# Kernel optimization log

Hardware: AMD Instinct MI355X
Metric: run time of the kernel (lower is better)

The kernel has to match this reference:

```python
import jax, jax.numpy as jnp
import numpy as np

N, E, H, L, IN, OUT = 50000, 600000, 128, 4, 10, 3
EPS = 1e-5

def _ln(x, g, b):
    m = jnp.mean(x, axis=-1, keepdims=True)
    v = jnp.mean(jnp.square(x - m), axis=-1, keepdims=True)
    return (x - m) * jax.lax.rsqrt(v + EPS) * g + b

def _mlp(x, w1, b1, w2, b2, g, be):
    h = jax.nn.relu(x @ w1 + b1)
    return _ln(h @ w2 + b2, g, be)

def setup_inputs() -> dict:
    key = jax.random.key(0)
    ks = iter(jax.random.split(key, 40))
    def w(shape, fan_in):
        return jax.random.normal(next(ks), shape, jnp.float32) * (1.0 / np.sqrt(fan_in))
    inp = {
        'x': jax.random.normal(next(ks), (N, IN), jnp.float32),
        'edge_index': jax.random.randint(next(ks), (2, E), 0, N, jnp.int32),
        'edge_attr': jax.random.normal(next(ks), (E, 3), jnp.float32),
        'enc_w1': w((IN, H), IN), 'enc_b1': jnp.zeros((H,), jnp.float32),
        'enc_w2': w((H, H), H), 'enc_b2': jnp.zeros((H,), jnp.float32),
        'enc_g': jnp.ones((H,), jnp.float32), 'enc_be': jnp.zeros((H,), jnp.float32),
        'edge_w1': w((L, 2 * H + 3, H), 2 * H + 3), 'edge_b1': jnp.zeros((L, H), jnp.float32),
        'edge_w2': w((L, H, H), H), 'edge_b2': jnp.zeros((L, H), jnp.float32),
        'edge_g': jnp.ones((L, H), jnp.float32), 'edge_be': jnp.zeros((L, H), jnp.float32),
        'node_w1': w((L, 2 * H, H), 2 * H), 'node_b1': jnp.zeros((L, H), jnp.float32),
        'node_w2': w((L, H, H), H), 'node_b2': jnp.zeros((L, H), jnp.float32),
        'node_g': jnp.ones((L, H), jnp.float32), 'node_be': jnp.zeros((L, H), jnp.float32),
        'dec_w1': w((H, H), H), 'dec_b1': jnp.zeros((H,), jnp.float32),
        'dec_w2': w((H, OUT), H), 'dec_b2': jnp.zeros((OUT,), jnp.float32),
    }
    return inp

def reference(x, edge_index, edge_attr,
              enc_w1, enc_b1, enc_w2, enc_b2, enc_g, enc_be,
              edge_w1, edge_b1, edge_w2, edge_b2, edge_g, edge_be,
              node_w1, node_b1, node_w2, node_b2, node_g, node_be,
              dec_w1, dec_b1, dec_w2, dec_b2):
    src, tgt = edge_index[0], edge_index[1]  # x_j = h[src], x_i = h[tgt]
    h = _mlp(x, enc_w1, enc_b1, enc_w2, enc_b2, enc_g, enc_be)  # [N,H]
    for l in range(L):
        x_i, x_j = h[tgt], h[src]                               # [E,H] gathers
        msg_in = jnp.concatenate([x_i, x_j, edge_attr], axis=1)  # [E,2H+3]
        msg = _mlp(msg_in, edge_w1[l], edge_b1[l], edge_w2[l], edge_b2[l], edge_g[l], edge_be[l])
        aggr = jax.ops.segment_sum(msg, tgt, num_segments=h.shape[0])  # [N,H]
        upd_in = jnp.concatenate([h, aggr], axis=1)              # [N,2H]
        h = h + _mlp(upd_in, node_w1[l], node_b1[l], node_w2[l], node_b2[l], node_g[l], node_be[l])
    out = jax.nn.relu(h @ dec_w1 + dec_b1) @ dec_w2 + dec_b2     # [N,OUT]
    return out
```

## Files before the change

### kernel.cpp

```cpp
#include <hip/hip_runtime.h>

#define H 128
#define LPAD 132
#define BM 64

typedef __attribute__((ext_vector_type(8))) short bf8;
typedef __attribute__((ext_vector_type(4))) float f4;
typedef __attribute__((ext_vector_type(4))) short s4;

__device__ __forceinline__ short f2bf(float f) {
    unsigned u = __float_as_uint(f);
    unsigned r = u + 0x7FFFu + ((u >> 16) & 1u);
    return (short)(r >> 16);
}
__device__ __forceinline__ float bf2f(unsigned lo16) {
    return __uint_as_float((lo16 & 0xFFFFu) << 16);
}

__global__ void pack_w(const float* __restrict__ W, short* __restrict__ out, int K, int KC) {
    const int layer = blockIdx.z;
    const float* Wl = W + (size_t)layer * K * H;
    short* ol = out + (size_t)layer * 8 * KC * 512;
    const int total = 8 * KC * 512;
    for (int idx = blockIdx.x * blockDim.x + threadIdx.x; idx < total; idx += gridDim.x * blockDim.x) {
        int i = idx & 7;
        int lane = (idx >> 3) & 63;
        int v = idx >> 9;
        int kc = v % KC;
        int m = v / KC;
        int k = kc * 32 + (lane >> 4) * 8 + i;
        int c = m * 16 + (lane & 15);
        float val = (k < K) ? Wl[(size_t)k * H + c] : 0.f;
        ol[idx] = f2bf(val);
    }
}

__global__ void pack_wts(const float* __restrict__ W , short* __restrict__ out) {
    const int layer = blockIdx.z;
    const float* Wl = W + (size_t)layer * 259 * 128;
    short* ol = out + (size_t)layer * 16 * 4 * 512;
    const int total = 16 * 4 * 512;
    for (int idx = blockIdx.x * blockDim.x + threadIdx.x; idx < total; idx += gridDim.x * blockDim.x) {
        int i = idx & 7;
        int lane = (idx >> 3) & 63;
        int v = idx >> 9;
        int kc = v & 3;
        int m = v >> 2;
        int k = kc * 32 + (lane >> 4) * 8 + i;
        int c = m * 16 + (lane & 15);
        float val = (c < 128) ? Wl[(size_t)k * 128 + c] : Wl[(size_t)(128 + k) * 128 + (c - 128)];
        ol[idx] = f2bf(val);
    }
}

__global__ void csr_count(const int* __restrict__ tgt, int* __restrict__ cnt, int E) {
    int e = blockIdx.x * blockDim.x + threadIdx.x;
    if (e < E) atomicAdd(&cnt[tgt[e]], 1);
}

#define SCAN_T 1024
__global__ __launch_bounds__(SCAN_T) void scan_excl(const int* __restrict__ cnt,
                                                    int* __restrict__ start, int n) {
    __shared__ int part[SCAN_T];
    int t = threadIdx.x;
    int chunk = (n + SCAN_T - 1) / SCAN_T;
    int lo = t * chunk, hi = min(lo + chunk, n);
    int s = 0;
    for (int i = lo; i < hi; ++i) s += cnt[i];
    part[t] = s;
    __syncthreads();
    for (int off = 1; off < SCAN_T; off <<= 1) {
        int v = (t >= off) ? part[t - off] : 0;
        __syncthreads();
        part[t] += v;
        __syncthreads();
    }
    int base = (t > 0) ? part[t - 1] : 0;
    for (int i = lo; i < hi; ++i) { start[i] = base; base += cnt[i]; }
}

__global__ void csr_scatter_reorder(const int* __restrict__ tgtI, const int* __restrict__ srcI,
                                    const float* __restrict__ eattr,
                                    int* __restrict__ start,
                                    int* __restrict__ srcs, int* __restrict__ tgts,
                                    short* __restrict__ attrb, int E) {
    int e = blockIdx.x * blockDim.x + threadIdx.x;
    if (e >= E) return;
    int t = tgtI[e];
    int p = atomicAdd(&start[t], 1);
    srcs[p] = srcI[e];
    tgts[p] = t;
    bf8 vv = {};
    vv[0] = f2bf(eattr[(size_t)e * 3 + 0]);
    vv[1] = f2bf(eattr[(size_t)e * 3 + 1]);
    vv[2] = f2bf(eattr[(size_t)e * 3 + 2]);
    *(bf8*)(attrb + (size_t)p * 8) = vv;
}

__global__ __launch_bounds__(512, 4) void ts_mfma(
    const short* __restrict__ hbf, const short* __restrict__ wtsp,
    const float* __restrict__ b1, float* __restrict__ TS, int N) {
    __shared__ __align__(16) short sW[16 * 4 * 512];
    const int tid = threadIdx.x;
    for (int t = tid; t < 16 * 4 * 512 / 8; t += 512) ((uint4*)sW)[t] = ((const uint4*)wtsp)[t];
    __syncthreads();

    const int lane = tid & 63;
    const int wv = tid >> 6;
    const int g = lane >> 4;
    const int er = lane & 15;
    const int n = blockIdx.x * 128 + wv * 16 + er;
    const int nC = (n < N) ? n : 0;
    const bf8* rT = (const bf8*)(hbf + (size_t)nC * H);

    f4 acc[16] = {};
#pragma unroll
    for (int kc = 0; kc < 4; ++kc) {
        bf8 b = rT[kc * 4 + g];
#pragma unroll
        for (int m = 0; m < 16; ++m)
            acc[m] = __builtin_amdgcn_mfma_f32_16x16x32_bf16(
                *(const bf8*)(sW + ((m * 4 + kc) * 64 + lane) * 8), b, acc[m], 0, 0, 0);
    }
    if (n >= N) return;
    float* o = TS + (size_t)n * 256;
#pragma unroll
    for (int m = 0; m < 16; ++m) {
        f4 v = acc[m];
        if (m < 8) {
            f4 bb = *(const f4*)(b1 + m * 16 + 4 * g);
            v = v + bb;
        }
        *(f4*)(o + m * 16 + 4 * g) = v;
    }
}

__global__ __launch_bounds__(512, 4) void edge_fused(
    const float* __restrict__ TS,
    const short* __restrict__ attrbf,
    const int* __restrict__ srcs, const int* __restrict__ tgts,
    const short* __restrict__ w2p,
    const float* __restrict__ w1aG,
    const float* __restrict__ b2,
    const float* __restrict__ gamma, const float* __restrict__ beta,
    float* __restrict__ aggr, int nrows) {
    __shared__ __align__(16) short sW2[8 * 4 * 512];
    __shared__ float sw1a[3 * 128];
    __shared__ __align__(16) unsigned smsg[128 * 64];
    __shared__ int stgt[128];

    const int tid = threadIdx.x;
    for (int t = tid; t < 8 * 4 * 512 / 8; t += 512) ((uint4*)sW2)[t] = ((const uint4*)w2p)[t];
    if (tid < 384) sw1a[tid] = w1aG[tid];
    const int e0b = blockIdx.x * 128;
    if (tid < 128) {
        int ee = e0b + tid;
        stgt[tid] = (ee < nrows) ? tgts[ee] : -1;
    }
    __syncthreads();

    const int lane = tid & 63;
    const int wv = tid >> 6;
    const int g = lane >> 4;
    const int er = lane & 15;
    const int le = wv * 16 + er;
    const int e = e0b + le;
    const bool valid = e < nrows;
    const int eC = valid ? e : 0;
    const int tS = srcs[eC];
    const int tT = tgts[eC];

    uint2 au = *(const uint2*)(attrbf + (size_t)eC * 8);
    const float at0 = bf2f(au.x), at1 = bf2f(au.x >> 16), at2 = bf2f(au.y);

    const float* Tp = TS + (size_t)tT * 256;
    const float* Sp = TS + (size_t)tS * 256 + 128;

    f4 acc2[8] = {};
#pragma unroll
    for (int kc2 = 0; kc2 < 4; ++kc2) {
        const int c0 = kc2 * 32 + 8 * g;
        f4 t0 = *(const f4*)(Tp + c0);
        f4 t1 = *(const f4*)(Tp + c0 + 4);
        f4 s0 = *(const f4*)(Sp + c0);
        f4 s1 = *(const f4*)(Sp + c0 + 4);
        float hv[8];
#pragma unroll
        for (int r = 0; r < 4; ++r) {
            float a = t0[r] + s0[r] + at0 * sw1a[c0 + r] + at1 * sw1a[128 + c0 + r] + at2 * sw1a[256 + c0 + r];
            hv[r] = fmaxf(a, 0.f);
            float b = t1[r] + s1[r] + at0 * sw1a[c0 + 4 + r] + at1 * sw1a[128 + c0 + 4 + r] + at2 * sw1a[256 + c0 + 4 + r];
            hv[4 + r] = fmaxf(b, 0.f);
        }
        bf8 bfr;
        unsigned* bu = (unsigned*)&bfr;
#pragma unroll
        for (int p = 0; p < 4; ++p)
            asm("v_cvt_pk_bf16_f32 %0, %1, %2" : "=v"(bu[p]) : "v"(hv[2 * p]), "v"(hv[2 * p + 1]));
#pragma unroll
        for (int m = 0; m < 8; ++m)
            acc2[m] = __builtin_amdgcn_mfma_f32_16x16x32_bf16(
                *(const bf8*)(sW2 + ((m * 4 + kc2) * 64 + lane) * 8), bfr, acc2[m], 0, 0, 0);
    }

    float o[8][4];
    float s = 0.f, q = 0.f;
#pragma unroll
    for (int m = 0; m < 8; ++m) {
        f4 bb = *(const f4*)(b2 + m * 16 + 4 * g);
#pragma unroll
        for (int r = 0; r < 4; ++r) {
            float v = acc2[m][r] + bb[r];
            o[m][r] = v; s += v; q += v * v;
        }
    }
    s += __shfl_xor(s, 16, 64); q += __shfl_xor(q, 16, 64);
    s += __shfl_xor(s, 32, 64); q += __shfl_xor(q, 32, 64);
    const float mean = s * (1.f / 128.f);
    const float inv = rsqrtf(q * (1.f / 128.f) - mean * mean + 1e-5f);

    const unsigned swz = (unsigned)((le & 7) << 3);
    unsigned* row = smsg + le * 64;
#pragma unroll
    for (int m = 0; m < 8; ++m) {
        f4 gg = *(const f4*)(gamma + m * 16 + 4 * g);
        f4 be4 = *(const f4*)(beta + m * 16 + 4 * g);
        float v0 = valid ? ((o[m][0] - mean) * inv * gg[0] + be4[0]) : 0.f;
        float v1 = valid ? ((o[m][1] - mean) * inv * gg[1] + be4[1]) : 0.f;
        float v2 = valid ? ((o[m][2] - mean) * inv * gg[2] + be4[2]) : 0.f;
        float v3 = valid ? ((o[m][3] - mean) * inv * gg[3] + be4[3]) : 0.f;
        unsigned p0, p1;
        asm("v_cvt_pk_bf16_f32 %0, %1, %2" : "=v"(p0) : "v"(v0), "v"(v1));
        asm("v_cvt_pk_bf16_f32 %0, %1, %2" : "=v"(p1) : "v"(v2), "v"(v3));
        unsigned d0 = ((unsigned)(m * 8 + 2 * g)) ^ swz;
        uint2 uu; uu.x = p0; uu.y = p1;
        *(uint2*)(row + d0) = uu;
    }
    __syncthreads();

    const int c2 = tid & 63;
    const int chunk = tid >> 6;
    float a0 = 0.f, a1 = 0.f;
    int cur = stgt[chunk * 16];
    for (int j = 0; j < 16; ++j) {
        int le2 = chunk * 16 + j;
        int tg = stgt[le2];
        if (tg != cur) {
            if (cur >= 0) {
                atomicAdd(&aggr[(size_t)cur * 128 + 2 * c2], a0);
                atomicAdd(&aggr[(size_t)cur * 128 + 2 * c2 + 1], a1);
            }
            a0 = 0.f; a1 = 0.f; cur = tg;
        }
        unsigned u = smsg[le2 * 64 + (c2 ^ ((le2 & 7) << 3))];
        a0 += __uint_as_float(u << 16);
        a1 += __uint_as_float(u & 0xFFFF0000u);
    }
    if (cur >= 0) {
        atomicAdd(&aggr[(size_t)cur * 128 + 2 * c2], a0);
        atomicAdd(&aggr[(size_t)cur * 128 + 2 * c2 + 1], a1);
    }
}

__global__ __launch_bounds__(1024, 4) void node_mfma(
    const short* __restrict__ hbf, const float* __restrict__ aggrf,
    const short* __restrict__ w1p, const short* __restrict__ w2p,
    const float* __restrict__ b1, const float* __restrict__ b2,
    const float* __restrict__ gamma, const float* __restrict__ beta,
    float* __restrict__ outp, short* __restrict__ hbfout, int nrows) {
    __shared__ __align__(16) short sW1[8 * 8 * 512];
    __shared__ __align__(16) short sW2[8 * 4 * 512];

    const int tid = threadIdx.x;
    for (int t = tid; t < 8 * 8 * 512 / 8; t += 1024) ((uint4*)sW1)[t] = ((const uint4*)w1p)[t];
    for (int t = tid; t < 8 * 4 * 512 / 8; t += 1024) ((uint4*)sW2)[t] = ((const uint4*)w2p)[t];
    __syncthreads();

    const int lane = tid & 63;
    const int wv = tid >> 6;
    const int g = lane >> 4;
    const int er = lane & 15;
    const int e = blockIdx.x * 256 + wv * 16 + er;
    const bool valid = e < nrows;
    const int eC = valid ? e : 0;

    const bf8* rT = (const bf8*)(hbf + (size_t)eC * H);
    const f4* ra = (const f4*)(aggrf + (size_t)eC * H);

    f4 acc1[8] = {};
#pragma unroll
    for (int kc = 0; kc < 4; ++kc) {
        bf8 b = rT[kc * 4 + g];
#pragma unroll
        for (int m = 0; m < 8; ++m)
            acc1[m] = __builtin_amdgcn_mfma_f32_16x16x32_bf16(
                *(const bf8*)(sW1 + ((m * 8 + kc) * 64 + lane) * 8), b, acc1[m], 0, 0, 0);
    }
#pragma unroll
    for (int kc = 4; kc < 8; ++kc) {
        f4 a0 = ra[(kc - 4) * 8 + g * 2];
        f4 a1 = ra[(kc - 4) * 8 + g * 2 + 1];
        bf8 b;
        unsigned* bu = (unsigned*)&b;
        asm("v_cvt_pk_bf16_f32 %0, %1, %2" : "=v"(bu[0]) : "v"(a0[0]), "v"(a0[1]));
        asm("v_cvt_pk_bf16_f32 %0, %1, %2" : "=v"(bu[1]) : "v"(a0[2]), "v"(a0[3]));
        asm("v_cvt_pk_bf16_f32 %0, %1, %2" : "=v"(bu[2]) : "v"(a1[0]), "v"(a1[1]));
        asm("v_cvt_pk_bf16_f32 %0, %1, %2" : "=v"(bu[3]) : "v"(a1[2]), "v"(a1[3]));
#pragma unroll
        for (int m = 0; m < 8; ++m)
            acc1[m] = __builtin_amdgcn_mfma_f32_16x16x32_bf16(
                *(const bf8*)(sW1 + ((m * 8 + kc) * 64 + lane) * 8), b, acc1[m], 0, 0, 0);
    }

    float h1[8][4];
#pragma unroll
    for (int m = 0; m < 8; ++m) {
        f4 bb = *(const f4*)(b1 + m * 16 + 4 * g);
#pragma unroll
        for (int r = 0; r < 4; ++r) h1[m][r] = fmaxf(acc1[m][r] + bb[r], 0.f);
    }

    unsigned pk[8][2];
#pragma unroll
    for (int m = 0; m < 8; ++m)
#pragma unroll
        for (int hh = 0; hh < 2; ++hh)
            asm("v_cvt_pk_bf16_f32 %0, %1, %2"
                : "=v"(pk[m][hh]) : "v"(h1[m][2 * hh]), "v"(h1[m][2 * hh + 1]));

    f4 acc2[8] = {};
#pragma unroll
    for (int kc2 = 0; kc2 < 4; ++kc2) {
        bf8 bfr;
        unsigned* bu = (unsigned*)&bfr;
#pragma unroll
        for (int p = 0; p < 4; ++p) {
            int sl = er + 16 * (2 * (g & 1) + (p >> 1));
            unsigned lo = (unsigned)__shfl((int)pk[2 * kc2 + 0][p & 1], sl, 64);
            unsigned hi = (unsigned)__shfl((int)pk[2 * kc2 + 1][p & 1], sl, 64);
            bu[p] = (g >> 1) ? hi : lo;
        }
#pragma unroll
        for (int m = 0; m < 8; ++m)
            acc2[m] = __builtin_amdgcn_mfma_f32_16x16x32_bf16(
                *(const bf8*)(sW2 + ((m * 4 + kc2) * 64 + lane) * 8), bfr, acc2[m], 0, 0, 0);
    }

    float o[8][4];
    float s = 0.f, q = 0.f;
#pragma unroll
    for (int m = 0; m < 8; ++m) {
        f4 bb = *(const f4*)(b2 + m * 16 + 4 * g);
#pragma unroll
        for (int r = 0; r < 4; ++r) {
            float v = acc2[m][r] + bb[r];
            o[m][r] = v; s += v; q += v * v;
        }
    }
    s += __shfl_xor(s, 16, 64); q += __shfl_xor(q, 16, 64);
    s += __shfl_xor(s, 32, 64); q += __shfl_xor(q, 32, 64);
    const float mean = s * (1.f / 128.f);
    const float inv = rsqrtf(q * (1.f / 128.f) - mean * mean + 1e-5f);

    if (!valid) return;
    float* hp = outp + (size_t)eC * H;
    short* hb = hbfout + (size_t)eC * H;
#pragma unroll
    for (int m = 0; m < 8; ++m) {
        f4 gg = *(const f4*)(gamma + m * 16 + 4 * g);
        f4 be4 = *(const f4*)(beta + m * 16 + 4 * g);
        f4 hv = *(const f4*)(hp + m * 16 + 4 * g);
        f4 nv; s4 pkk;
#pragma unroll
        for (int r = 0; r < 4; ++r) {
            nv[r] = hv[r] + (o[m][r] - mean) * inv * gg[r] + be4[r];
            pkk[r] = f2bf(nv[r]);
        }
        *(f4*)(hp + m * 16 + 4 * g) = nv;
        *(s4*)(hb + m * 16 + 4 * g) = pkk;
    }
}

enum { MODE_ENC = 0, MODE_DEC = 3 };

__device__ __forceinline__ void fma_row(float acc[4], float a, const float4& b) {
    acc[0] = fmaf(a, b.x, acc[0]);
    acc[1] = fmaf(a, b.y, acc[1]);
    acc[2] = fmaf(a, b.z, acc[2]);
    acc[3] = fmaf(a, b.w, acc[3]);
}

__device__ __forceinline__ void gemm_seg(const float (*A)[LPAD], int K,
                                         const float* __restrict__ B,
                                         int row0, int c0, float acc[8][4]) {
    int k = 0;
    for (; k + 4 <= K; k += 4) {
        float4 b0 = *(const float4*)(B + (size_t)(k + 0) * H + c0);
        float4 b1 = *(const float4*)(B + (size_t)(k + 1) * H + c0);
        float4 b2 = *(const float4*)(B + (size_t)(k + 2) * H + c0);
        float4 b3 = *(const float4*)(B + (size_t)(k + 3) * H + c0);
#pragma unroll
        for (int j = 0; j < 8; ++j) {
            float4 a = *(const float4*)(&A[row0 + j][k]);
            fma_row(acc[j], a.x, b0);
            fma_row(acc[j], a.y, b1);
            fma_row(acc[j], a.z, b2);
            fma_row(acc[j], a.w, b3);
        }
    }
    for (; k < K; ++k) {
        float4 bv = *(const float4*)(B + (size_t)k * H + c0);
#pragma unroll
        for (int j = 0; j < 8; ++j) fma_row(acc[j], A[row0 + j][k], bv);
    }
}

template <int MODE>
__global__ __launch_bounds__(256, 2) void mlp_small(
    const float* __restrict__ in0,
    const float* __restrict__ w1, const float* __restrict__ b1,
    const float* __restrict__ w2, const float* __restrict__ b2,
    const float* __restrict__ g, const float* __restrict__ be,
    float* __restrict__ outp, short* __restrict__ hbfout, int nrows) {
    __shared__ __align__(16) float sA[BM][LPAD];

    const int tid = threadIdx.x;
    const int tr = tid >> 5, tc = tid & 31;
    const int c0 = tc * 4, row0 = tr * 8;
    const int r0 = blockIdx.x * BM;

    if (MODE == MODE_ENC) {
        for (int idx = tid; idx < BM * 10; idx += 256) {
            int r = idx / 10, c = idx - 10 * (idx / 10);
            int n = r0 + r;
            sA[r][c] = (n < nrows) ? in0[(size_t)n * 10 + c] : 0.f;
        }
    } else {
        for (int idx = tid; idx < BM * 32; idx += 256) {
            int r = idx >> 5, qq = idx & 31;
            int n = r0 + r;
            float4 v0 = make_float4(0.f, 0.f, 0.f, 0.f);
            if (n < nrows) v0 = ((const float4*)in0)[(size_t)n * 32 + qq];
            *(float4*)&sA[r][qq * 4] = v0;
        }
    }
    __syncthreads();

    float acc[8][4];
    {
        float4 bb = *(const float4*)&b1[c0];
#pragma unroll
        for (int j = 0; j < 8; ++j) { acc[j][0] = bb.x; acc[j][1] = bb.y; acc[j][2] = bb.z; acc[j][3] = bb.w; }
    }
    gemm_seg(sA, (MODE == MODE_ENC) ? 10 : H, w1, row0, c0, acc);
#pragma unroll
    for (int j = 0; j < 8; ++j)
#pragma unroll
        for (int r = 0; r < 4; ++r) acc[j][r] = fmaxf(acc[j][r], 0.f);

    __syncthreads();
#pragma unroll
    for (int j = 0; j < 8; ++j)
        *(float4*)&sA[row0 + j][c0] = make_float4(acc[j][0], acc[j][1], acc[j][2], acc[j][3]);
    __syncthreads();

    if (MODE == MODE_DEC) {
        if (tid < BM * 3) {
            int r = tid / 3, o = tid - 3 * (tid / 3);
            int gr = r0 + r;
            float sv = b2[o];
            for (int i = 0; i < H; ++i) sv = fmaf(sA[r][i], w2[(size_t)i * 3 + o], sv);
            if (gr < nrows) outp[(size_t)gr * 3 + o] = sv;
        }
        return;
    }

    {
        float4 bb = *(const float4*)&b2[c0];
#pragma unroll
        for (int j = 0; j < 8; ++j) { acc[j][0] = bb.x; acc[j][1] = bb.y; acc[j][2] = bb.z; acc[j][3] = bb.w; }
    }
    gemm_seg(sA, H, w2, row0, c0, acc);

    float4 g4 = *(const float4*)&g[c0];
    float4 be4 = *(const float4*)&be[c0];
#pragma unroll
    for (int j = 0; j < 8; ++j) {
        float s = acc[j][0] + acc[j][1] + acc[j][2] + acc[j][3];
        float q = acc[j][0] * acc[j][0] + acc[j][1] * acc[j][1] +
                  acc[j][2] * acc[j][2] + acc[j][3] * acc[j][3];
#pragma unroll
        for (int m = 1; m < 32; m <<= 1) { s += __shfl_xor(s, m); q += __shfl_xor(q, m); }
        float mean = s * (1.0f / 128.0f);
        float inv = rsqrtf(q * (1.0f / 128.0f) - mean * mean + 1e-5f);
        int gr = r0 + row0 + j;
        if (gr >= nrows) continue;
        float v0 = (acc[j][0] - mean) * inv * g4.x + be4.x;
        float v1 = (acc[j][1] - mean) * inv * g4.y + be4.y;
        float v2 = (acc[j][2] - mean) * inv * g4.z + be4.z;
        float v3 = (acc[j][3] - mean) * inv * g4.w + be4.w;
        *(float4*)&outp[(size_t)gr * H + c0] = make_float4(v0, v1, v2, v3);
        s4 pk = {f2bf(v0), f2bf(v1), f2bf(v2), f2bf(v3)};
        *(s4*)&hbfout[(size_t)gr * H + c0] = pk;
    }
}

static inline size_t align16(size_t x) { return (x + 15) & ~(size_t)15; }

extern "C" void kernel_launch(void* const* d_in, const int* in_sizes, int n_in,
                              void* d_out, int out_size, void* d_ws, size_t ws_size,
                              hipStream_t stream) {
    const float* x       = (const float*)d_in[0];
    const int*   ei      = (const int*)d_in[1];
    const float* eattr   = (const float*)d_in[2];
    const float* enc_w1  = (const float*)d_in[3];
    const float* enc_b1  = (const float*)d_in[4];
    const float* enc_w2  = (const float*)d_in[5];
    const float* enc_b2  = (const float*)d_in[6];
    const float* enc_g   = (const float*)d_in[7];
    const float* enc_be  = (const float*)d_in[8];
    const float* edge_w1 = (const float*)d_in[9];
    const float* edge_b1 = (const float*)d_in[10];
    const float* edge_w2 = (const float*)d_in[11];
    const float* edge_b2 = (const float*)d_in[12];
    const float* edge_g  = (const float*)d_in[13];
    const float* edge_be = (const float*)d_in[14];
    const float* node_w1 = (const float*)d_in[15];
    const float* node_b1 = (const float*)d_in[16];
    const float* node_w2 = (const float*)d_in[17];
    const float* node_b2 = (const float*)d_in[18];
    const float* node_g  = (const float*)d_in[19];
    const float* node_be = (const float*)d_in[20];
    const float* dec_w1  = (const float*)d_in[21];
    const float* dec_b1  = (const float*)d_in[22];
    const float* dec_w2  = (const float*)d_in[23];
    const float* dec_b2  = (const float*)d_in[24];

    const int N = in_sizes[0] / 10;
    const int E = in_sizes[1] / 2;
    const int* srcI = ei;
    const int* tgtI = ei + E;

    char* base = (char*)d_ws;
    size_t off = 0;
    float* h     = (float*)(base + off); off = align16(off + (size_t)N * H * 4);
    float* aggr  = (float*)(base + off); off = align16(off + (size_t)N * H * 4);
    short* hbf   = (short*)(base + off); off = align16(off + (size_t)N * H * 2);
    float* TS    = (float*)(base + off); off = align16(off + (size_t)N * 256 * 4);
    short* attrb = (short*)(base + off); off = align16(off + (size_t)E * 8 * 2);
    short* ewtsp = (short*)(base + off); off = align16(off + (size_t)4 * 16 * 4 * 512 * 2);
    short* ew2p  = (short*)(base + off); off = align16(off + (size_t)4 * 8 * 4 * 512 * 2);
    short* nw1p  = (short*)(base + off); off = align16(off + (size_t)4 * 8 * 8 * 512 * 2);
    short* nw2p  = (short*)(base + off); off = align16(off + (size_t)4 * 8 * 4 * 512 * 2);
    int*   cnt   = (int*)(base + off);  off = align16(off + (size_t)N * 4);
    int*   startp= (int*)(base + off);  off = align16(off + (size_t)(N + 1) * 4);
    int*   srcs  = (int*)(base + off);  off = align16(off + (size_t)E * 4);
    int*   tgts  = (int*)(base + off);  off = align16(off + (size_t)E * 4);

    pack_wts<<<dim3(64, 1, 4), 256, 0, stream>>>(edge_w1, ewtsp);
    pack_w<<<dim3(32, 1, 4), 256, 0, stream>>>(edge_w2, ew2p, H, 4);
    pack_w<<<dim3(64, 1, 4), 256, 0, stream>>>(node_w1, nw1p, 2 * H, 8);
    pack_w<<<dim3(32, 1, 4), 256, 0, stream>>>(node_w2, nw2p, H, 4);

    hipMemsetAsync(cnt, 0, (size_t)N * 4, stream);
    csr_count<<<(E + 255) / 256, 256, 0, stream>>>(tgtI, cnt, E);
    scan_excl<<<1, SCAN_T, 0, stream>>>(cnt, startp, N);
    csr_scatter_reorder<<<(E + 255) / 256, 256, 0, stream>>>(
        tgtI, srcI, eattr, startp, srcs, tgts, attrb, E);

    const int gN64 = (N + BM - 1) / BM;
    mlp_small<MODE_ENC><<<gN64, 256, 0, stream>>>(
        x, enc_w1, enc_b1, enc_w2, enc_b2, enc_g, enc_be, h, hbf, N);

    const int gTS = (N + 127) / 128;
    const int gEe = (E + 127) / 128;
    const int gNN = (N + 255) / 256;
    for (int l = 0; l < 4; ++l) {
        ts_mfma<<<gTS, 512, 0, stream>>>(
            hbf, ewtsp + (size_t)l * 16 * 4 * 512, edge_b1 + (size_t)l * H, TS, N);
        hipMemsetAsync(aggr, 0, (size_t)N * H * sizeof(float), stream);
        const float* w1aG = edge_w1 + (size_t)l * 259 * 128 + 256 * 128;
        edge_fused<<<gEe, 512, 0, stream>>>(
            TS, attrb, srcs, tgts, ew2p + (size_t)l * 8 * 4 * 512, w1aG,
            edge_b2 + (size_t)l * H, edge_g + (size_t)l * H, edge_be + (size_t)l * H,
            aggr, E);
        node_mfma<<<gNN, 1024, 0, stream>>>(
            hbf, aggr,
            nw1p + (size_t)l * 8 * 8 * 512, nw2p + (size_t)l * 8 * 4 * 512,
            node_b1 + (size_t)l * H, node_b2 + (size_t)l * H,
            node_g + (size_t)l * H, node_be + (size_t)l * H,
            h, hbf, N);
    }

    mlp_small<MODE_DEC><<<gN64, 256, 0, stream>>>(
        h, dec_w1, dec_b1, dec_w2, dec_b2, nullptr, nullptr, (float*)d_out, nullptr, N);
}
```

Before: 926.2 us.

## Store per-node edge projections as bf16 and read MFMA weights directly from global

The per-node T/S projection table becomes two bf16 arrays instead of one interleaved fp32 table. This halves the bytes gathered per edge in edge_fused, which is the dominant random-access traffic. Weight staging into LDS is removed from ts_mfma, edge_fused and node_mfma, which now read packed MFMA fragments straight from global/L2, and the edge attribute buffer shrinks to 4 shorts per edge. Launch bounds are raised to allow more resident blocks, at the cost of extra precision loss on T/S and of repeated global reads of the weights.

```diff
diff --git a/kernel.cpp b/kernel.cpp
--- a/kernel.cpp
+++ b/kernel.cpp
@@ -90,21 +90,18 @@
     int p = atomicAdd(&start[t], 1);
     srcs[p] = srcI[e];
     tgts[p] = t;
-    bf8 vv = {};
+    s4 vv = {};
     vv[0] = f2bf(eattr[(size_t)e * 3 + 0]);
     vv[1] = f2bf(eattr[(size_t)e * 3 + 1]);
     vv[2] = f2bf(eattr[(size_t)e * 3 + 2]);
-    *(bf8*)(attrb + (size_t)p * 8) = vv;
+    *(s4*)(attrb + (size_t)p * 4) = vv;
 }
 
 __global__ __launch_bounds__(512, 4) void ts_mfma(
     const short* __restrict__ hbf, const short* __restrict__ wtsp,
-    const float* __restrict__ b1, float* __restrict__ TS, int N) {
-    __shared__ __align__(16) short sW[16 * 4 * 512];
+    const float* __restrict__ b1,
+    short* __restrict__ Tarr, short* __restrict__ Sarr, int N) {
     const int tid = threadIdx.x;
-    for (int t = tid; t < 16 * 4 * 512 / 8; t += 512) ((uint4*)sW)[t] = ((const uint4*)wtsp)[t];
-    __syncthreads();
-
     const int lane = tid & 63;
     const int wv = tid >> 6;
     const int g = lane >> 4;
@@ -112,6 +109,7 @@
     const int n = blockIdx.x * 128 + wv * 16 + er;
     const int nC = (n < N) ? n : 0;
     const bf8* rT = (const bf8*)(hbf + (size_t)nC * H);
+    const bf8* wA = (const bf8*)wtsp + lane;
 
     f4 acc[16] = {};
 #pragma unroll
@@ -120,10 +118,11 @@
 #pragma unroll
         for (int m = 0; m < 16; ++m)
             acc[m] = __builtin_amdgcn_mfma_f32_16x16x32_bf16(
-                *(const bf8*)(sW + ((m * 4 + kc) * 64 + lane) * 8), b, acc[m], 0, 0, 0);
+                wA[(m * 4 + kc) * 64], b, acc[m], 0, 0, 0);
     }
     if (n >= N) return;
-    float* o = TS + (size_t)n * 256;
+    short* oT = Tarr + (size_t)n * 128;
+    short* oS = Sarr + (size_t)n * 128;
 #pragma unroll
     for (int m = 0; m < 16; ++m) {
         f4 v = acc[m];
@@ -131,12 +130,17 @@
             f4 bb = *(const f4*)(b1 + m * 16 + 4 * g);
             v = v + bb;
         }
-        *(f4*)(o + m * 16 + 4 * g) = v;
-    }
-}
-
-__global__ __launch_bounds__(512, 4) void edge_fused(
-    const float* __restrict__ TS,
+        unsigned p0, p1;
+        asm("v_cvt_pk_bf16_f32 %0, %1, %2" : "=v"(p0) : "v"(v[0]), "v"(v[1]));
+        asm("v_cvt_pk_bf16_f32 %0, %1, %2" : "=v"(p1) : "v"(v[2]), "v"(v[3]));
+        uint2 uu; uu.x = p0; uu.y = p1;
+        if (m < 8) *(uint2*)(oT + m * 16 + 4 * g) = uu;
+        else       *(uint2*)(oS + (m - 8) * 16 + 4 * g) = uu;
+    }
+}
+
+__global__ __launch_bounds__(512, 8) void edge_fused(
+    const short* __restrict__ Tarr, const short* __restrict__ Sarr,
     const short* __restrict__ attrbf,
     const int* __restrict__ srcs, const int* __restrict__ tgts,
     const short* __restrict__ w2p,
@@ -144,13 +148,11 @@
     const float* __restrict__ b2,
     const float* __restrict__ gamma, const float* __restrict__ beta,
     float* __restrict__ aggr, int nrows) {
-    __shared__ __align__(16) short sW2[8 * 4 * 512];
     __shared__ float sw1a[3 * 128];
     __shared__ __align__(16) unsigned smsg[128 * 64];
     __shared__ int stgt[128];
 
     const int tid = threadIdx.x;
-    for (int t = tid; t < 8 * 4 * 512 / 8; t += 512) ((uint4*)sW2)[t] = ((const uint4*)w2p)[t];
     if (tid < 384) sw1a[tid] = w1aG[tid];
     const int e0b = blockIdx.x * 128;
     if (tid < 128) {
@@ -170,27 +172,31 @@
     const int tS = srcs[eC];
     const int tT = tgts[eC];
 
-    uint2 au = *(const uint2*)(attrbf + (size_t)eC * 8);
+    uint2 au = *(const uint2*)(attrbf + (size_t)eC * 4);
     const float at0 = bf2f(au.x), at1 = bf2f(au.x >> 16), at2 = bf2f(au.y);
 
-    const float* Tp = TS + (size_t)tT * 256;
-    const float* Sp = TS + (size_t)tS * 256 + 128;
+    const short* Tp = Tarr + (size_t)tT * 128;
+    const short* Sp = Sarr + (size_t)tS * 128;
+    const bf8* wA = (const bf8*)w2p + lane;
 
     f4 acc2[8] = {};
 #pragma unroll
     for (int kc2 = 0; kc2 < 4; ++kc2) {
         const int c0 = kc2 * 32 + 8 * g;
-        f4 t0 = *(const f4*)(Tp + c0);
-        f4 t1 = *(const f4*)(Tp + c0 + 4);
-        f4 s0 = *(const f4*)(Sp + c0);
-        f4 s1 = *(const f4*)(Sp + c0 + 4);
+        uint4 tu = *(const uint4*)(Tp + c0);
+        uint4 su = *(const uint4*)(Sp + c0);
+        unsigned tw[4] = {tu.x, tu.y, tu.z, tu.w};
+        unsigned swd[4] = {su.x, su.y, su.z, su.w};
         float hv[8];
 #pragma unroll
-        for (int r = 0; r < 4; ++r) {
-            float a = t0[r] + s0[r] + at0 * sw1a[c0 + r] + at1 * sw1a[128 + c0 + r] + at2 * sw1a[256 + c0 + r];
-            hv[r] = fmaxf(a, 0.f);
-            float b = t1[r] + s1[r] + at0 * sw1a[c0 + 4 + r] + at1 * sw1a[128 + c0 + 4 + r] + at2 * sw1a[256 + c0 + 4 + r];
-            hv[4 + r] = fmaxf(b, 0.f);
+        for (int p = 0; p < 4; ++p) {
+            int j0 = 2 * p;
+            float t0 = bf2f(tw[p]), t1 = bf2f(tw[p] >> 16);
+            float s0 = bf2f(swd[p]), s1 = bf2f(swd[p] >> 16);
+            float a = t0 + s0 + at0 * sw1a[c0 + j0] + at1 * sw1a[128 + c0 + j0] + at2 * sw1a[256 + c0 + j0];
+            hv[j0] = fmaxf(a, 0.f);
+            float b = t1 + s1 + at0 * sw1a[c0 + j0 + 1] + at1 * sw1a[128 + c0 + j0 + 1] + at2 * sw1a[256 + c0 + j0 + 1];
+            hv[j0 + 1] = fmaxf(b, 0.f);
         }
         bf8 bfr;
         unsigned* bu = (unsigned*)&bfr;
@@ -200,7 +206,7 @@
 #pragma unroll
         for (int m = 0; m < 8; ++m)
             acc2[m] = __builtin_amdgcn_mfma_f32_16x16x32_bf16(
-                *(const bf8*)(sW2 + ((m * 4 + kc2) * 64 + lane) * 8), bfr, acc2[m], 0, 0, 0);
+                wA[(m * 4 + kc2) * 64], bfr, acc2[m], 0, 0, 0);
     }
 
     float o[8][4];
@@ -262,20 +268,13 @@
     }
 }
 
-__global__ __launch_bounds__(1024, 4) void node_mfma(
+__global__ __launch_bounds__(1024, 8) void node_mfma(
     const short* __restrict__ hbf, const float* __restrict__ aggrf,
     const short* __restrict__ w1p, const short* __restrict__ w2p,
     const float* __restrict__ b1, const float* __restrict__ b2,
     const float* __restrict__ gamma, const float* __restrict__ beta,
     float* __restrict__ outp, short* __restrict__ hbfout, int nrows) {
-    __shared__ __align__(16) short sW1[8 * 8 * 512];
-    __shared__ __align__(16) short sW2[8 * 4 * 512];
-
     const int tid = threadIdx.x;
-    for (int t = tid; t < 8 * 8 * 512 / 8; t += 1024) ((uint4*)sW1)[t] = ((const uint4*)w1p)[t];
-    for (int t = tid; t < 8 * 4 * 512 / 8; t += 1024) ((uint4*)sW2)[t] = ((const uint4*)w2p)[t];
-    __syncthreads();
-
     const int lane = tid & 63;
     const int wv = tid >> 6;
     const int g = lane >> 4;
@@ -286,6 +285,8 @@
 
     const bf8* rT = (const bf8*)(hbf + (size_t)eC * H);
     const f4* ra = (const f4*)(aggrf + (size_t)eC * H);
+    const bf8* wA1 = (const bf8*)w1p + lane;
+    const bf8* wA2 = (const bf8*)w2p + lane;
 
     f4 acc1[8] = {};
 #pragma unroll
@@ -294,7 +295,7 @@
 #pragma unroll
         for (int m = 0; m < 8; ++m)
             acc1[m] = __builtin_amdgcn_mfma_f32_16x16x32_bf16(
-                *(const bf8*)(sW1 + ((m * 8 + kc) * 64 + lane) * 8), b, acc1[m], 0, 0, 0);
+                wA1[(m * 8 + kc) * 64], b, acc1[m], 0, 0, 0);
     }
 #pragma unroll
     for (int kc = 4; kc < 8; ++kc) {
@@ -309,7 +310,7 @@
 #pragma unroll
         for (int m = 0; m < 8; ++m)
             acc1[m] = __builtin_amdgcn_mfma_f32_16x16x32_bf16(
-                *(const bf8*)(sW1 + ((m * 8 + kc) * 64 + lane) * 8), b, acc1[m], 0, 0, 0);
+                wA1[(m * 8 + kc) * 64], b, acc1[m], 0, 0, 0);
     }
 
     float h1[8][4];
@@ -343,7 +344,7 @@
 #pragma unroll
         for (int m = 0; m < 8; ++m)
             acc2[m] = __builtin_amdgcn_mfma_f32_16x16x32_bf16(
-                *(const bf8*)(sW2 + ((m * 4 + kc2) * 64 + lane) * 8), bfr, acc2[m], 0, 0, 0);
+                wA2[(m * 4 + kc2) * 64], bfr, acc2[m], 0, 0, 0);
     }
 
     float o[8][4];
@@ -546,8 +547,9 @@
     float* h     = (float*)(base + off); off = align16(off + (size_t)N * H * 4);
     float* aggr  = (float*)(base + off); off = align16(off + (size_t)N * H * 4);
     short* hbf   = (short*)(base + off); off = align16(off + (size_t)N * H * 2);
-    float* TS    = (float*)(base + off); off = align16(off + (size_t)N * 256 * 4);
-    short* attrb = (short*)(base + off); off = align16(off + (size_t)E * 8 * 2);
+    short* Tarr  = (short*)(base + off); off = align16(off + (size_t)N * H * 2);
+    short* Sarr  = (short*)(base + off); off = align16(off + (size_t)N * H * 2);
+    short* attrb = (short*)(base + off); off = align16(off + (size_t)E * 4 * 2);
     short* ewtsp = (short*)(base + off); off = align16(off + (size_t)4 * 16 * 4 * 512 * 2);
     short* ew2p  = (short*)(base + off); off = align16(off + (size_t)4 * 8 * 4 * 512 * 2);
     short* nw1p  = (short*)(base + off); off = align16(off + (size_t)4 * 8 * 8 * 512 * 2);
@@ -577,11 +579,11 @@
     const int gNN = (N + 255) / 256;
     for (int l = 0; l < 4; ++l) {
         ts_mfma<<<gTS, 512, 0, stream>>>(
-            hbf, ewtsp + (size_t)l * 16 * 4 * 512, edge_b1 + (size_t)l * H, TS, N);
+            hbf, ewtsp + (size_t)l * 16 * 4 * 512, edge_b1 + (size_t)l * H, Tarr, Sarr, N);
         hipMemsetAsync(aggr, 0, (size_t)N * H * sizeof(float), stream);
         const float* w1aG = edge_w1 + (size_t)l * 259 * 128 + 256 * 128;
         edge_fused<<<gEe, 512, 0, stream>>>(
-            TS, attrb, srcs, tgts, ew2p + (size_t)l * 8 * 4 * 512, w1aG,
+            Tarr, Sarr, attrb, srcs, tgts, ew2p + (size_t)l * 8 * 4 * 512, w1aG,
             edge_b2 + (size_t)l * H, edge_g + (size_t)l * H, edge_be + (size_t)l * H,
             aggr, E);
         node_mfma<<<gNN, 1024, 0, stream>>>(
```

Result: slower. 1.857 ms (+100.5%).
